# Kernel optimization log

Measured on AMD Instinct MI355X. Metric: run time of the kernel, lower is better.

## Reference

```python
import jax, jax.numpy as jnp
import numpy as np

B, N, D = 32, 512, 256
ITERATION_STEPS = 2


def setup_inputs() -> dict:
    key = jax.random.key(0)
    ks = jax.random.split(key, 20)
    node = jax.random.normal(ks[0], (B, N, D), dtype=jnp.float32)
    node_mask = jnp.ones((B, N), dtype=jnp.int32)
    graphs = [(jax.random.uniform(ks[1 + i], (B, N, N)) < 0.05).astype(jnp.int32)
              for i in range(6)]
    s = 0.02
    params = {
        'w_nw': jax.random.normal(ks[8], (D, 1)) * s,
        'b_nw': jnp.zeros((1,), jnp.float32),
        'w_self': jax.random.normal(ks[9], (D, D)) * s,
        'b_self': jnp.zeros((D,), jnp.float32),
        'w_arg1': jax.random.normal(ks[10], (D, D)) * s,
        'w_arg2': jax.random.normal(ks[11], (D, D)) * s,
        'w_arg3': jax.random.normal(ks[12], (D, D)) * s,
        'w_arg4': jax.random.normal(ks[13], (D, D)) * s,
        'w_punct': jax.random.normal(ks[14], (D, D)) * s,
        'w_punct_re': jax.random.normal(ks[15], (D, D)) * s,
    }
    return {'node': node, 'node_mask': node_mask,
            'arg_graph_1': graphs[0], 'arg_graph_2': graphs[1],
            'arg_graph_3': graphs[2], 'arg_graph_4': graphs[3],
            'punct_graph': graphs[4], 'punct_graph_re': graphs[5],
            **params}


def reference(node, node_mask, arg_graph_1, arg_graph_2, arg_graph_3, arg_graph_4,
              punct_graph, punct_graph_re,
              w_nw, b_nw, w_self, b_self,
              w_arg1, w_arg2, w_arg3, w_arg4, w_punct, w_punct_re):
    n = node.shape[1]
    diag = jnp.eye(n, dtype=node_mask.dtype)  # [N,N]
    # dd_graph: pairwise valid mask with zeroed diagonal, [B,N,N]
    dd = node_mask[:, None, :] * node_mask[:, :, None] * (1 - diag)
    G = jnp.stack([arg_graph_1, arg_graph_2, arg_graph_3, arg_graph_4,
                   punct_graph, punct_graph_re], 0) * dd[None]  # [6,B,N,N]
    Gf = G.astype(node.dtype)
    # neighbor count over all 6 edge types; replace 0 by 1 to avoid div-by-zero
    nn_num = Gf.sum(axis=(0, -1))  # [B,N]
    nn_num = jnp.where(nn_num >= 1, nn_num, jnp.ones_like(nn_num))
    W = jnp.stack([w_arg1, w_arg2, w_arg3, w_arg4, w_punct, w_punct_re], 0)  # [6,D,D]

    all_weight = []
    for _ in range(ITERATION_STEPS):
        # (1) node relatedness measure
        d_node_weight = jax.nn.sigmoid(node @ w_nw + b_nw)[..., 0]  # [B,N]
        all_weight.append(d_node_weight)
        self_node_info = node @ w_self + b_self  # [B,N,D]
        # (2) message propagation: per edge type k, project then aggregate
        proj = jnp.einsum('bnd,kde->kbne', node, W)            # [6,B,N,D]
        masked_w = d_node_weight[None, :, None, :] * Gf        # [6,B,N,N]
        agg = jnp.einsum('kbmn,kbne->bme', masked_w, proj)     # [B,N,D]
        # (3) update
        node = jax.nn.relu(self_node_info + agg / nn_num[..., None])
    return node, jnp.stack(all_weight, axis=1)  # [B,N,D], [B,steps,N]
```

## Files before the change

### kernel.cpp

```cpp
#include <hip/hip_runtime.h>

#define Bb 32
#define Nn 512
#define Dd 256
#define KC 1792
#define NR (Bb * Nn)

typedef __bf16 bf16x8 __attribute__((ext_vector_type(8)));
typedef float  f32x4  __attribute__((ext_vector_type(4)));
typedef int    i32x4  __attribute__((ext_vector_type(4)));
typedef unsigned short u16;

__device__ __forceinline__ u16 f2bf(float x){
  union { float f; unsigned u; } c; c.f = x;
  unsigned u = c.u;
  u += 0x7FFFu + ((u >> 16) & 1u);
  return (u16)(u >> 16);
}

__global__ __launch_bounds__(256) void k_prep(
    const float* __restrict__ wself,
    const float* __restrict__ w0, const float* __restrict__ w1,
    const float* __restrict__ w2, const float* __restrict__ w3,
    const float* __restrict__ w4, const float* __restrict__ w5,
    u16* __restrict__ wcatT){
  int e = blockIdx.x;
  const float* Ws[7] = {wself, w0, w1, w2, w3, w4, w5};
  for (int c = threadIdx.x; c < KC; c += 256){
    int g = c >> 8, j = c & 255;
    wcatT[(size_t)e*KC + c] = f2bf(Ws[g][j*Dd + e]);
  }
}

#define GLD(d, p, o) asm volatile("global_load_dwordx4 %0, %1, off offset:" #o \
                                  : "=v"(d) : "v"(p))

__global__ __launch_bounds__(256) void k_pack(
    const int* __restrict__ g0, const int* __restrict__ g1,
    const int* __restrict__ g2, const int* __restrict__ g3,
    const int* __restrict__ g4, const int* __restrict__ g5,
    const int* __restrict__ mask,
    unsigned* __restrict__ Gp, float* __restrict__ rs){
  int t = threadIdx.x, l = t & 63, wv = t >> 6;
  int r = blockIdx.x * 4 + wv;
  int b = r >> 9, m = r & 511;
  size_t off = (size_t)r * Nn + l * 4;
  const int* pm = mask + (size_t)b * Nn + l * 4;
  const int* pa = g0 + off; const int* pb = g1 + off; const int* pcx = g2 + off;
  const int* pd = g3 + off; const int* pe = g4 + off; const int* pf = g5 + off;

  i32x4 A0,A1,B0,B1,C0,C1,D0,D1,E0,E1,F0,F1,M0,M1;
  GLD(M0,pm,0);  GLD(M1,pm,1024);
  GLD(A0,pa,0);  GLD(A1,pa,1024);
  GLD(B0,pb,0);  GLD(B1,pb,1024);
  GLD(C0,pcx,0); GLD(C1,pcx,1024);
  GLD(D0,pd,0);  GLD(D1,pd,1024);
  GLD(E0,pe,0);  GLD(E1,pe,1024);
  GLD(F0,pf,0);  GLD(F1,pf,1024);
  asm volatile("s_waitcnt vmcnt(0)" ::: "memory");
  __builtin_amdgcn_sched_barrier(0);

  int s1 = (l & 1) * 4, s2 = ((l >> 1) & 1) * 8, s3 = ((l >> 2) & 1) * 16;
  unsigned dm0 = ((m >> 2) == l)      ? (1u << (m & 3)) : 0u;
  unsigned dm1 = ((m >> 2) == 64 + l) ? (1u << (m & 3)) : 0u;
  int stot = 0;
#define PK(G, MM, DM, k, h) {                                              \
    unsigned nib = (unsigned)((G[0] & MM[0]) | ((G[1] & MM[1]) << 1) |     \
                              ((G[2] & MM[2]) << 2) | ((G[3] & MM[3]) << 3)) \
                   & ~(DM);                                                \
    stot += __popc(nib);                                                   \
    unsigned v = nib << s1; v |= (unsigned)__shfl_xor((int)v, 1);          \
    v <<= s2;               v |= (unsigned)__shfl_xor((int)v, 2);          \
    v <<= s3;               v |= (unsigned)__shfl_xor((int)v, 4);          \
    if ((l & 7) == 0)                                                      \
      Gp[((size_t)(k) * NR + r) * 16 + (h) * 8 + (l >> 3)] = v; }
  PK(A0,M0,dm0,0,0) PK(A1,M1,dm1,0,1)
  PK(B0,M0,dm0,1,0) PK(B1,M1,dm1,1,1)
  PK(C0,M0,dm0,2,0) PK(C1,M1,dm1,2,1)
  PK(D0,M0,dm0,3,0) PK(D1,M1,dm1,3,1)
  PK(E0,M0,dm0,4,0) PK(E1,M1,dm1,4,1)
  PK(F0,M0,dm0,5,0) PK(F1,M1,dm1,5,1)
#undef PK
  #pragma unroll
  for (int o = 1; o < 64; o <<= 1) stot += __shfl_xor(stot, o);
  if (l == 0)
    rs[r] = mask[r] ? 1.0f / (float)(stot < 1 ? 1 : stot) : 0.0f;
}
#undef GLD

__global__ __launch_bounds__(256) void k_dw(
    const float* __restrict__ node, const int* __restrict__ mask,
    const float* __restrict__ wnw, const float* __restrict__ bnw,
    float* __restrict__ aw_out,
    u16* __restrict__ Nbf, u16* __restrict__ Xp){
  __shared__ float tile[32][268];
  __shared__ float dws[32];
  int b = blockIdx.x >> 4, n0 = (blockIdx.x & 15) << 5;
  int t = threadIdx.x;
  int row = t >> 3, seg = t & 7;
  const float* src = node + ((size_t)(b * Nn + n0 + row)) * Dd + seg * 32;
  u16* zn = Nbf + ((size_t)(b * Nn + n0 + row)) * Dd + seg * 32;
  #pragma unroll
  for (int c = 0; c < 8; ++c){
    float4 v = ((const float4*)src)[c];
    tile[row][seg * 32 + c * 4 + 0] = v.x;
    tile[row][seg * 32 + c * 4 + 1] = v.y;
    tile[row][seg * 32 + c * 4 + 2] = v.z;
    tile[row][seg * 32 + c * 4 + 3] = v.w;
    ushort4 h;
    h.x = f2bf(v.x); h.y = f2bf(v.y); h.z = f2bf(v.z); h.w = f2bf(v.w);
    ((ushort4*)zn)[c] = h;
  }
  __syncthreads();
  float s = 0.f;
  #pragma unroll
  for (int c = 0; c < 32; ++c) s += tile[row][seg * 32 + c] * wnw[seg * 32 + c];
  s += __shfl_xor(s, 1); s += __shfl_xor(s, 2); s += __shfl_xor(s, 4);
  if (seg == 0){
    float dw = 1.f / (1.f + expf(-(s + bnw[0])));
    aw_out[b * (2 * Nn) + n0 + row] = dw;
    dws[row] = mask[b * Nn + n0 + row] ? dw : 0.f;
  }
  __syncthreads();
  {
    float dwr = dws[row];
    u16* xp = Xp + ((size_t)(b * Nn + n0 + row)) * Dd + seg * 32;
    #pragma unroll
    for (int c = 0; c < 8; ++c){
      ushort4 h;
      h.x = f2bf(dwr * tile[row][seg * 32 + c * 4 + 0]);
      h.y = f2bf(dwr * tile[row][seg * 32 + c * 4 + 1]);
      h.z = f2bf(dwr * tile[row][seg * 32 + c * 4 + 2]);
      h.w = f2bf(dwr * tile[row][seg * 32 + c * 4 + 3]);
      ((ushort4*)xp)[c] = h;
    }
  }
}

__global__ __launch_bounds__(256) void k_ycat(
    const u16* __restrict__ Xp, const u16* __restrict__ wcatT,
    u16* __restrict__ Yt){
  int n0 = blockIdx.x * 128, c0 = blockIdx.y * 128, b = blockIdx.z;
  int kg = c0 >> 8, eg0 = c0 & 255;
  __shared__ u16 As[128 * 72];
  __shared__ u16 Bs[128 * 72];
  int t = threadIdx.x, lane = t & 63, wid = t >> 6;
  int wm = wid >> 1, wn = wid & 1;
  f32x4 acc[4][4];
  #pragma unroll
  for (int i = 0; i < 4; ++i)
    #pragma unroll
    for (int q = 0; q < 4; ++q) acc[i][q] = (f32x4){0.f, 0.f, 0.f, 0.f};

  for (int ks = 0; ks < 4; ++ks){
    int k0 = ks * 64;
    #pragma unroll
    for (int p = 0; p < 4; ++p){
      int row = p * 32 + (t >> 3);
      *(uint4*)&As[row * 72 + (t & 7) * 8] =
          *(const uint4*)(Xp + ((size_t)(b * Nn + n0 + row)) * Dd + k0 + (t & 7) * 8);
      *(uint4*)&Bs[row * 72 + (t & 7) * 8] =
          *(const uint4*)(wcatT + (size_t)(eg0 + row) * KC + 256 + kg * 256 + k0 + (t & 7) * 8);
    }
    __syncthreads();
    #pragma unroll
    for (int kk = 0; kk < 2; ++kk){
      bf16x8 av[4], bv[4];
      #pragma unroll
      for (int i = 0; i < 4; ++i)
        av[i] = *(const bf16x8*)&As[(wm * 64 + i * 16 + (lane & 15)) * 72 + kk * 32 + (lane >> 4) * 8];
      #pragma unroll
      for (int q = 0; q < 4; ++q)
        bv[q] = *(const bf16x8*)&Bs[(wn * 64 + q * 16 + (lane & 15)) * 72 + kk * 32 + (lane >> 4) * 8];
      #pragma unroll
      for (int i = 0; i < 4; ++i)
        #pragma unroll
        for (int q = 0; q < 4; ++q)
          acc[i][q] = __builtin_amdgcn_mfma_f32_16x16x32_bf16(av[i], bv[q], acc[i][q], 0, 0, 0);
    }
    __syncthreads();
  }
  #pragma unroll
  for (int i = 0; i < 4; ++i){
    int nbase = n0 + wm * 64 + i * 16 + (lane >> 4) * 4;
    #pragma unroll
    for (int q = 0; q < 4; ++q){
      int eg = eg0 + wn * 64 + q * 16 + (lane & 15);
      ushort4 h;
      h.x = f2bf(acc[i][q][0]); h.y = f2bf(acc[i][q][1]);
      h.z = f2bf(acc[i][q][2]); h.w = f2bf(acc[i][q][3]);
      *(ushort4*)(Yt + ((size_t)((b * 6 + kg) * 256 + eg)) * Nn + nbase) = h;
    }
  }
}

__global__ __launch_bounds__(256) void k_agg2(
    const unsigned* __restrict__ Gp, const u16* __restrict__ Yt,
    const u16* __restrict__ Nbf, const u16* __restrict__ wcatT,
    const float* __restrict__ rs, const float* __restrict__ bself,
    float* __restrict__ outp){
  __shared__ u16 As[64 * 72];
  __shared__ u16 BW[128 * 72];
  int id = blockIdx.x;
  int xcd = id & 7, q = id >> 3;
  int b = xcd * 4 + (q & 3), mt = (q >> 2) & 7, z = q >> 5;
  int m0 = mt * 64, e0 = z * 128;
  int t = threadIdx.x, lane = t & 63, wn = t >> 6;
  int arow = t >> 2, aq = t & 3;

  float rsv[16];
  #pragma unroll
  for (int i = 0; i < 4; ++i)
    #pragma unroll
    for (int r = 0; r < 4; ++r)
      rsv[i * 4 + r] = rs[b * Nn + m0 + i * 16 + (lane >> 4) * 4 + r];

  f32x4 accA[4][2], accS[4][2];
  #pragma unroll
  for (int i = 0; i < 4; ++i)
    #pragma unroll
    for (int q2 = 0; q2 < 2; ++q2){
      accA[i][q2] = (f32x4){0.f, 0.f, 0.f, 0.f};
      accS[i][q2] = (f32x4){0.f, 0.f, 0.f, 0.f};
    }

  for (int k = 0; k < 6; ++k){
    const unsigned* Gr = Gp + ((size_t)k * NR + b * Nn + m0) * 16;
    unsigned wpre[8];
    #pragma unroll
    for (int ks2 = 0; ks2 < 8; ++ks2)
      wpre[ks2] = Gr[arow * 16 + ks2 * 2 + (aq >> 1)];
    const u16* Yk = Yt + ((size_t)((b * 6 + k) * 256)) * Nn;

    for (int ks2 = 0; ks2 < 8; ++ks2){
      {
        unsigned bits = (wpre[ks2] >> ((aq & 1) * 16)) & 0xFFFFu;
        union { u16 h[16]; uint4 v[2]; } pk;
        #pragma unroll
        for (int c = 0; c < 16; ++c)
          pk.h[c] = ((bits >> c) & 1u) ? 0x3F80 : 0;
        *(uint4*)&As[arow * 72 + aq * 16]     = pk.v[0];
        *(uint4*)&As[arow * 72 + aq * 16 + 8] = pk.v[1];
      }
      #pragma unroll
      for (int p = 0; p < 4; ++p){
        int rowb = p * 32 + (t >> 3);
        *(uint4*)&BW[rowb * 72 + (t & 7) * 8] =
            *(const uint4*)(Yk + (size_t)(e0 + rowb) * Nn + ks2 * 64 + (t & 7) * 8);
      }
      __syncthreads();
      #pragma unroll
      for (int kk = 0; kk < 2; ++kk){
        bf16x8 av[4], bv[2];
        #pragma unroll
        for (int i = 0; i < 4; ++i)
          av[i] = *(const bf16x8*)&As[(i * 16 + (lane & 15)) * 72 + kk * 32 + (lane >> 4) * 8];
        #pragma unroll
        for (int q2 = 0; q2 < 2; ++q2)
          bv[q2] = *(const bf16x8*)&BW[(wn * 32 + q2 * 16 + (lane & 15)) * 72 + kk * 32 + (lane >> 4) * 8];
        #pragma unroll
        for (int i = 0; i < 4; ++i)
          #pragma unroll
          for (int q2 = 0; q2 < 2; ++q2)
            accA[i][q2] = __builtin_amdgcn_mfma_f32_16x16x32_bf16(av[i], bv[q2], accA[i][q2], 0, 0, 0);
      }
      __syncthreads();
    }
  }
  for (int ds = 0; ds < 4; ++ds){
    #pragma unroll
    for (int p = 0; p < 2; ++p){
      int row = p * 32 + (t >> 3);
      *(uint4*)&As[row * 72 + (t & 7) * 8] =
          *(const uint4*)(Nbf + ((size_t)(b * Nn + m0 + row)) * Dd + ds * 64 + (t & 7) * 8);
    }
    #pragma unroll
    for (int p = 0; p < 4; ++p){
      int rowb = p * 32 + (t >> 3);
      *(uint4*)&BW[rowb * 72 + (t & 7) * 8] =
          *(const uint4*)(wcatT + (size_t)(e0 + rowb) * KC + ds * 64 + (t & 7) * 8);
    }
    __syncthreads();
    #pragma unroll
    for (int kk = 0; kk < 2; ++kk){
      bf16x8 av[4], bv[2];
      #pragma unroll
      for (int i = 0; i < 4; ++i)
        av[i] = *(const bf16x8*)&As[(i * 16 + (lane & 15)) * 72 + kk * 32 + (lane >> 4) * 8];
      #pragma unroll
      for (int q2 = 0; q2 < 2; ++q2)
        bv[q2] = *(const bf16x8*)&BW[(wn * 32 + q2 * 16 + (lane & 15)) * 72 + kk * 32 + (lane >> 4) * 8];
      #pragma unroll
      for (int i = 0; i < 4; ++i)
        #pragma unroll
        for (int q2 = 0; q2 < 2; ++q2)
          accS[i][q2] = __builtin_amdgcn_mfma_f32_16x16x32_bf16(av[i], bv[q2], accS[i][q2], 0, 0, 0);
    }
    __syncthreads();
  }
  #pragma unroll
  for (int i = 0; i < 4; ++i){
    #pragma unroll
    for (int r = 0; r < 4; ++r){
      size_t gr = (size_t)b * Nn + m0 + i * 16 + (lane >> 4) * 4 + r;
      float rsm = rsv[i * 4 + r];
      #pragma unroll
      for (int q2 = 0; q2 < 2; ++q2){
        int col = e0 + wn * 32 + q2 * 16 + (lane & 15);
        float v = rsm * accA[i][q2][r] + accS[i][q2][r] + bself[col];
        outp[gr * Dd + col] = v > 0.f ? v : 0.f;
      }
    }
  }
}

extern "C" void kernel_launch(void* const* d_in, const int* in_sizes, int n_in,
                              void* d_out, int out_size, void* d_ws, size_t ws_size,
                              hipStream_t stream){
  (void)in_sizes; (void)n_in; (void)out_size; (void)ws_size;
  const float* node  = (const float*)d_in[0];
  const int*   mask  = (const int*)d_in[1];
  const int*   g[6];
  for (int i = 0; i < 6; ++i) g[i] = (const int*)d_in[2 + i];
  const float* wnw   = (const float*)d_in[8];
  const float* bnw   = (const float*)d_in[9];
  const float* wself = (const float*)d_in[10];
  const float* bself = (const float*)d_in[11];
  const float* W[6];
  for (int i = 0; i < 6; ++i) W[i] = (const float*)d_in[12 + i];

  float* out_node = (float*)d_out;
  float* out_aw   = out_node + (size_t)Bb * Nn * Dd;

  char* ws = (char*)d_ws;
  u16*      wcatT = (u16*)(ws);
  float*    rs    = (float*)(ws + 917504);
  unsigned* Gp    = (unsigned*)(ws + 1048576);
  u16*      Xp    = (u16*)(ws + 7340032);
  u16*      Nbf   = (u16*)(ws + 15728640);
  u16*      Yt    = (u16*)(ws + 24117248);

  k_prep<<<256, 256, 0, stream>>>(wself, W[0], W[1], W[2], W[3], W[4], W[5], wcatT);
  k_pack<<<4096, 256, 0, stream>>>(g[0], g[1], g[2], g[3], g[4], g[5], mask, Gp, rs);

  for (int t = 0; t < 2; ++t){
    const float* nsrc = (t == 0) ? node : out_node;
    k_dw<<<512, 256, 0, stream>>>(nsrc, mask, wnw, bnw, out_aw + t * Nn, Nbf, Xp);
    k_ycat<<<dim3(4, 12, 32), 256, 0, stream>>>(Xp, wcatT, Yt);
    k_agg2<<<512, 256, 0, stream>>>(Gp, Yt, Nbf, wcatT, rs, bself, out_node);
  }
}
```

Baseline: 243.4 us.

## Fuse graph bit-packing into first-iteration aggregation kernel

Removes the standalone graph packing kernel and folds the packing, neighbor counting and row-scale computation into a new first-step aggregation kernel that reads the raw int32 adjacencies directly and writes the packed bits for the second step. It also merges the aggregation and self-projection accumulators by pre-scaling the aggregate before the self GEMM, saving registers. The intent is to avoid a separate pass and launch over the large adjacency data; the first-step kernel uses a smaller row tile and loads all 256 output columns per block.

```diff
diff --git a/kernel.cpp b/kernel.cpp
--- a/kernel.cpp
+++ b/kernel.cpp
@@ -31,62 +31,6 @@
     wcatT[(size_t)e*KC + c] = f2bf(Ws[g][j*Dd + e]);
   }
 }
-
-#define GLD(d, p, o) asm volatile("global_load_dwordx4 %0, %1, off offset:" #o \
-                                  : "=v"(d) : "v"(p))
-
-__global__ __launch_bounds__(256) void k_pack(
-    const int* __restrict__ g0, const int* __restrict__ g1,
-    const int* __restrict__ g2, const int* __restrict__ g3,
-    const int* __restrict__ g4, const int* __restrict__ g5,
-    const int* __restrict__ mask,
-    unsigned* __restrict__ Gp, float* __restrict__ rs){
-  int t = threadIdx.x, l = t & 63, wv = t >> 6;
-  int r = blockIdx.x * 4 + wv;
-  int b = r >> 9, m = r & 511;
-  size_t off = (size_t)r * Nn + l * 4;
-  const int* pm = mask + (size_t)b * Nn + l * 4;
-  const int* pa = g0 + off; const int* pb = g1 + off; const int* pcx = g2 + off;
-  const int* pd = g3 + off; const int* pe = g4 + off; const int* pf = g5 + off;
-
-  i32x4 A0,A1,B0,B1,C0,C1,D0,D1,E0,E1,F0,F1,M0,M1;
-  GLD(M0,pm,0);  GLD(M1,pm,1024);
-  GLD(A0,pa,0);  GLD(A1,pa,1024);
-  GLD(B0,pb,0);  GLD(B1,pb,1024);
-  GLD(C0,pcx,0); GLD(C1,pcx,1024);
-  GLD(D0,pd,0);  GLD(D1,pd,1024);
-  GLD(E0,pe,0);  GLD(E1,pe,1024);
-  GLD(F0,pf,0);  GLD(F1,pf,1024);
-  asm volatile("s_waitcnt vmcnt(0)" ::: "memory");
-  __builtin_amdgcn_sched_barrier(0);
-
-  int s1 = (l & 1) * 4, s2 = ((l >> 1) & 1) * 8, s3 = ((l >> 2) & 1) * 16;
-  unsigned dm0 = ((m >> 2) == l)      ? (1u << (m & 3)) : 0u;
-  unsigned dm1 = ((m >> 2) == 64 + l) ? (1u << (m & 3)) : 0u;
-  int stot = 0;
-#define PK(G, MM, DM, k, h) {                                              \
-    unsigned nib = (unsigned)((G[0] & MM[0]) | ((G[1] & MM[1]) << 1) |     \
-                              ((G[2] & MM[2]) << 2) | ((G[3] & MM[3]) << 3)) \
-                   & ~(DM);                                                \
-    stot += __popc(nib);                                                   \
-    unsigned v = nib << s1; v |= (unsigned)__shfl_xor((int)v, 1);          \
-    v <<= s2;               v |= (unsigned)__shfl_xor((int)v, 2);          \
-    v <<= s3;               v |= (unsigned)__shfl_xor((int)v, 4);          \
-    if ((l & 7) == 0)                                                      \
-      Gp[((size_t)(k) * NR + r) * 16 + (h) * 8 + (l >> 3)] = v; }
-  PK(A0,M0,dm0,0,0) PK(A1,M1,dm1,0,1)
-  PK(B0,M0,dm0,1,0) PK(B1,M1,dm1,1,1)
-  PK(C0,M0,dm0,2,0) PK(C1,M1,dm1,2,1)
-  PK(D0,M0,dm0,3,0) PK(D1,M1,dm1,3,1)
-  PK(E0,M0,dm0,4,0) PK(E1,M1,dm1,4,1)
-  PK(F0,M0,dm0,5,0) PK(F1,M1,dm1,5,1)
-#undef PK
-  #pragma unroll
-  for (int o = 1; o < 64; o <<= 1) stot += __shfl_xor(stot, o);
-  if (l == 0)
-    rs[r] = mask[r] ? 1.0f / (float)(stot < 1 ? 1 : stot) : 0.0f;
-}
-#undef GLD
 
 __global__ __launch_bounds__(256) void k_dw(
     const float* __restrict__ node, const int* __restrict__ mask,
@@ -190,6 +134,158 @@
       h.x = f2bf(acc[i][q][0]); h.y = f2bf(acc[i][q][1]);
       h.z = f2bf(acc[i][q][2]); h.w = f2bf(acc[i][q][3]);
       *(ushort4*)(Yt + ((size_t)((b * 6 + kg) * 256 + eg)) * Nn + nbase) = h;
+    }
+  }
+}
+
+__global__ __launch_bounds__(256) void k_agg1(
+    const int* __restrict__ g0, const int* __restrict__ g1,
+    const int* __restrict__ g2, const int* __restrict__ g3,
+    const int* __restrict__ g4, const int* __restrict__ g5,
+    const int* __restrict__ mask, const u16* __restrict__ Yt,
+    const u16* __restrict__ Nbf, const u16* __restrict__ wcatT,
+    const float* __restrict__ bself,
+    unsigned char* __restrict__ Gp8, float* __restrict__ rs,
+    float* __restrict__ outp){
+  __shared__ u16 As[32 * 72];
+  __shared__ u16 BW[256 * 72];
+  __shared__ int nns[32][9];
+  __shared__ float rsl[32];
+  __shared__ unsigned char lmask8[64];
+  const int* gs[6] = {g0, g1, g2, g3, g4, g5};
+  int id = blockIdx.x;
+  int xcd = id & 7, q = id >> 3;
+  int b = xcd * 4 + (q & 3), mt = q >> 2;
+  int m0 = mt * 32;
+  int t = threadIdx.x, lane = t & 63, wn = t >> 6;
+  int arow = t >> 3, q8 = t & 7;
+  int mloc = m0 + arow;
+
+  if (t < 64){
+    const int* mp = mask + (size_t)b * Nn + t * 8;
+    unsigned mb = 0;
+    #pragma unroll
+    for (int j = 0; j < 8; ++j) mb |= (unsigned)(mp[j] & 1) << j;
+    lmask8[t] = (unsigned char)mb;
+  }
+  __syncthreads();
+
+  f32x4 acc[2][4];
+  #pragma unroll
+  for (int i = 0; i < 2; ++i)
+    #pragma unroll
+    for (int q2 = 0; q2 < 4; ++q2) acc[i][q2] = (f32x4){0.f, 0.f, 0.f, 0.f};
+
+  int nnp = 0;
+  for (int k = 0; k < 6; ++k){
+    const int* Gk = gs[k] + ((size_t)(b * Nn + m0)) * Nn;
+    const u16* Yk = Yt + ((size_t)((b * 6 + k) * 256)) * Nn;
+    for (int ks = 0; ks < 8; ++ks){
+      {
+        const i32x4* gp = (const i32x4*)(Gk + (size_t)arow * Nn + ks * 64 + q8 * 8);
+        i32x4 x0 = gp[0], x1 = gp[1];
+        unsigned bits = (unsigned)((x0[0] & 1) | ((x0[1] & 1) << 1) |
+                                   ((x0[2] & 1) << 2) | ((x0[3] & 1) << 3) |
+                                   ((x1[0] & 1) << 4) | ((x1[1] & 1) << 5) |
+                                   ((x1[2] & 1) << 6) | ((x1[3] & 1) << 7));
+        unsigned dm = ((mloc >> 3) == (ks * 8 + q8)) ? (1u << (mloc & 7)) : 0u;
+        bits &= ~dm;
+        unsigned mb = lmask8[ks * 8 + q8];
+        unsigned bm = bits & mb;
+        nnp += __popc(bm);
+        Gp8[(((size_t)k * NR + b * Nn + m0 + arow) * 16 + ks * 2 + (q8 >> 2)) * 4 + (q8 & 3)] =
+            (unsigned char)bm;
+        union { u16 h[8]; uint4 v; } pk;
+        #pragma unroll
+        for (int c = 0; c < 8; ++c)
+          pk.h[c] = ((bits >> c) & 1u) ? 0x3F80 : 0;
+        *(uint4*)&As[arow * 72 + q8 * 8] = pk.v;
+      }
+      #pragma unroll
+      for (int p = 0; p < 8; ++p){
+        int rowb = p * 32 + (t >> 3);
+        *(uint4*)&BW[rowb * 72 + (t & 7) * 8] =
+            *(const uint4*)(Yk + (size_t)rowb * Nn + ks * 64 + (t & 7) * 8);
+      }
+      __syncthreads();
+      #pragma unroll
+      for (int kk = 0; kk < 2; ++kk){
+        bf16x8 av[2], bv[4];
+        #pragma unroll
+        for (int i = 0; i < 2; ++i)
+          av[i] = *(const bf16x8*)&As[(i * 16 + (lane & 15)) * 72 + kk * 32 + (lane >> 4) * 8];
+        #pragma unroll
+        for (int q2 = 0; q2 < 4; ++q2)
+          bv[q2] = *(const bf16x8*)&BW[(wn * 64 + q2 * 16 + (lane & 15)) * 72 + kk * 32 + (lane >> 4) * 8];
+        #pragma unroll
+        for (int i = 0; i < 2; ++i)
+          #pragma unroll
+          for (int q2 = 0; q2 < 4; ++q2)
+            acc[i][q2] = __builtin_amdgcn_mfma_f32_16x16x32_bf16(av[i], bv[q2], acc[i][q2], 0, 0, 0);
+      }
+      __syncthreads();
+    }
+  }
+  nns[arow][q8] = nnp;
+  __syncthreads();
+  if (t < 32){
+    int s = 0;
+    #pragma unroll
+    for (int j = 0; j < 8; ++j) s += nns[t][j];
+    int r = b * Nn + m0 + t;
+    float v = mask[r] ? 1.0f / (float)(s < 1 ? 1 : s) : 0.0f;
+    rsl[t] = v;
+    rs[r] = v;
+  }
+  __syncthreads();
+  #pragma unroll
+  for (int i = 0; i < 2; ++i)
+    #pragma unroll
+    for (int rr = 0; rr < 4; ++rr){
+      float s = rsl[i * 16 + (lane >> 4) * 4 + rr];
+      #pragma unroll
+      for (int q2 = 0; q2 < 4; ++q2) acc[i][q2][rr] *= s;
+    }
+  for (int ds = 0; ds < 4; ++ds){
+    if (t < 256){
+      *(uint4*)&As[(t >> 3) * 72 + (t & 7) * 8] =
+          *(const uint4*)(Nbf + ((size_t)(b * Nn + m0 + (t >> 3))) * Dd + ds * 64 + (t & 7) * 8);
+    }
+    #pragma unroll
+    for (int p = 0; p < 8; ++p){
+      int rowb = p * 32 + (t >> 3);
+      *(uint4*)&BW[rowb * 72 + (t & 7) * 8] =
+          *(const uint4*)(wcatT + (size_t)rowb * KC + ds * 64 + (t & 7) * 8);
+    }
+    __syncthreads();
+    #pragma unroll
+    for (int kk = 0; kk < 2; ++kk){
+      bf16x8 av[2], bv[4];
+      #pragma unroll
+      for (int i = 0; i < 2; ++i)
+        av[i] = *(const bf16x8*)&As[(i * 16 + (lane & 15)) * 72 + kk * 32 + (lane >> 4) * 8];
+      #pragma unroll
+      for (int q2 = 0; q2 < 4; ++q2)
+        bv[q2] = *(const bf16x8*)&BW[(wn * 64 + q2 * 16 + (lane & 15)) * 72 + kk * 32 + (lane >> 4) * 8];
+      #pragma unroll
+      for (int i = 0; i < 2; ++i)
+        #pragma unroll
+        for (int q2 = 0; q2 < 4; ++q2)
+          acc[i][q2] = __builtin_amdgcn_mfma_f32_16x16x32_bf16(av[i], bv[q2], acc[i][q2], 0, 0, 0);
+    }
+    __syncthreads();
+  }
+  #pragma unroll
+  for (int i = 0; i < 2; ++i){
+    #pragma unroll
+    for (int rr = 0; rr < 4; ++rr){
+      size_t gr = (size_t)b * Nn + m0 + i * 16 + (lane >> 4) * 4 + rr;
+      #pragma unroll
+      for (int q2 = 0; q2 < 4; ++q2){
+        int col = wn * 64 + q2 * 16 + (lane & 15);
+        float v = acc[i][q2][rr] + bself[col];
+        outp[gr * Dd + col] = v > 0.f ? v : 0.f;
+      }
     }
   }
 }
@@ -215,14 +311,12 @@
     for (int r = 0; r < 4; ++r)
       rsv[i * 4 + r] = rs[b * Nn + m0 + i * 16 + (lane >> 4) * 4 + r];
 
-  f32x4 accA[4][2], accS[4][2];
+  f32x4 accA[4][2];
   #pragma unroll
   for (int i = 0; i < 4; ++i)
     #pragma unroll
-    for (int q2 = 0; q2 < 2; ++q2){
+    for (int q2 = 0; q2 < 2; ++q2)
       accA[i][q2] = (f32x4){0.f, 0.f, 0.f, 0.f};
-      accS[i][q2] = (f32x4){0.f, 0.f, 0.f, 0.f};
-    }
 
   for (int k = 0; k < 6; ++k){
     const unsigned* Gr = Gp + ((size_t)k * NR + b * Nn + m0) * 16;
@@ -267,6 +361,14 @@
       __syncthreads();
     }
   }
+  #pragma unroll
+  for (int i = 0; i < 4; ++i)
+    #pragma unroll
+    for (int rr = 0; rr < 4; ++rr){
+      float s = rsv[i * 4 + rr];
+      #pragma unroll
+      for (int q2 = 0; q2 < 2; ++q2) accA[i][q2][rr] *= s;
+    }
   for (int ds = 0; ds < 4; ++ds){
     #pragma unroll
     for (int p = 0; p < 2; ++p){
@@ -294,20 +396,19 @@
       for (int i = 0; i < 4; ++i)
         #pragma unroll
         for (int q2 = 0; q2 < 2; ++q2)
-          accS[i][q2] = __builtin_amdgcn_mfma_f32_16x16x32_bf16(av[i], bv[q2], accS[i][q2], 0, 0, 0);
+          accA[i][q2] = __builtin_amdgcn_mfma_f32_16x16x32_bf16(av[i], bv[q2], accA[i][q2], 0, 0, 0);
     }
     __syncthreads();
   }
   #pragma unroll
   for (int i = 0; i < 4; ++i){
     #pragma unroll
-    for (int r = 0; r < 4; ++r){
-      size_t gr = (size_t)b * Nn + m0 + i * 16 + (lane >> 4) * 4 + r;
-      float rsm = rsv[i * 4 + r];
+    for (int rr = 0; rr < 4; ++rr){
+      size_t gr = (size_t)b * Nn + m0 + i * 16 + (lane >> 4) * 4 + rr;
       #pragma unroll
       for (int q2 = 0; q2 < 2; ++q2){
         int col = e0 + wn * 32 + q2 * 16 + (lane & 15);
-        float v = rsm * accA[i][q2][r] + accS[i][q2][r] + bself[col];
+        float v = accA[i][q2][rr] + bself[col];
         outp[gr * Dd + col] = v > 0.f ? v : 0.f;
       }
     }
@@ -341,12 +442,14 @@
   u16*      Yt    = (u16*)(ws + 24117248);
 
   k_prep<<<256, 256, 0, stream>>>(wself, W[0], W[1], W[2], W[3], W[4], W[5], wcatT);
-  k_pack<<<4096, 256, 0, stream>>>(g[0], g[1], g[2], g[3], g[4], g[5], mask, Gp, rs);
-
-  for (int t = 0; t < 2; ++t){
-    const float* nsrc = (t == 0) ? node : out_node;
-    k_dw<<<512, 256, 0, stream>>>(nsrc, mask, wnw, bnw, out_aw + t * Nn, Nbf, Xp);
-    k_ycat<<<dim3(4, 12, 32), 256, 0, stream>>>(Xp, wcatT, Yt);
-    k_agg2<<<512, 256, 0, stream>>>(Gp, Yt, Nbf, wcatT, rs, bself, out_node);
-  }
-}
+
+  k_dw<<<512, 256, 0, stream>>>(node, mask, wnw, bnw, out_aw, Nbf, Xp);
+  k_ycat<<<dim3(4, 12, 32), 256, 0, stream>>>(Xp, wcatT, Yt);
+  k_agg1<<<512, 256, 0, stream>>>(g[0], g[1], g[2], g[3], g[4], g[5], mask,
+                                  Yt, Nbf, wcatT, bself,
+                                  (unsigned char*)Gp, rs, out_node);
+
+  k_dw<<<512, 256, 0, stream>>>(out_node, mask, wnw, bnw, out_aw + Nn, Nbf, Xp);
+  k_ycat<<<dim3(4, 12, 32), 256, 0, stream>>>(Xp, wcatT, Yt);
+  k_agg2<<<512, 256, 0, stream>>>(Gp, Yt, Nbf, wcatT, rs, bself, out_node);
+}
```

Result: no change. 242.5 us (median of 2 runs) (-0.4%).
